# Performance work log

Hardware: AMD Instinct MI355X
Metric: run time of the kernel (lower is better)

Reference implementation:

```python
import jax, jax.numpy as jnp
import numpy as np

B, D, U = 64, 256, 256

def setup_inputs() -> dict:
    key = jax.random.key(0)
    ks = jax.random.split(key, 16)
    init_mu = 0.05
    inputs = jax.random.normal(ks[0], (B, D), jnp.float32)
    prev_state = 0.1 * jax.random.normal(ks[1], (B, U), jnp.float32)
    A = jax.random.normal(ks[2], (B, U, U), jnp.float32)
    # symmetric, diagonally boosted covariance-like state
    Sigma_state = 0.01 * (A + jnp.swapaxes(A, 1, 2)) + 0.1 * jnp.eye(U, dtype=jnp.float32)
    def w(k, shape):
        return init_mu * jax.random.normal(k, shape, jnp.float32)
    def s(k):
        return jax.random.uniform(k, (U,), jnp.float32, -4.5, -2.2)
    return {
        'inputs': inputs, 'prev_state': prev_state, 'Sigma_state': Sigma_state,
        'U_z': w(ks[3], (D, U)), 'uz_sigma': s(ks[4]), 'W_z': w(ks[5], (U, U)), 'wz_sigma': s(ks[6]),
        'U_r': w(ks[7], (D, U)), 'ur_sigma': s(ks[8]), 'W_r': w(ks[9], (U, U)), 'wr_sigma': s(ks[10]),
        'U_h': w(ks[11], (D, U)), 'uh_sigma': s(ks[12]), 'W_h': w(ks[13], (U, U)), 'wh_sigma': s(ks[14]),
    }

def _outer(a, b):  # [B,u],[B,u] -> [B,u,u]
    return a[:, :, None] * b[:, None, :]

def _quad(W, S):  # W^T @ S @ W, S is [B,u,u]
    return jnp.matmul(jnp.matmul(W.T, S), W)

def _x_sigma_w(x, sv):  # ||x||^2 * diag(softplus sigma)
    return jnp.sum(x * x, axis=1)[:, None, None] * jnp.diag(sv)

def _tr_sigma_w(S, sv):  # trace(S) * diag(softplus sigma)
    return jnp.trace(S, axis1=1, axis2=2)[:, None, None] * jnp.diag(sv)

def _hadamard_sigma(S1, S2, m1, m2):
    # S1*S2 + diag(m1) S2 diag(m1) + diag(m2) S1 diag(m2) as elementwise/broadcast
    return S1 * S2 + _outer(m1, m1) * S2 + _outer(m2, m2) * S1

def reference(inputs, prev_state, Sigma_state, U_z, uz_sigma, W_z, wz_sigma,
              U_r, ur_sigma, W_r, wr_sigma, U_h, uh_sigma, W_h, wh_sigma):
    sp = jax.nn.softplus
    # --- z gate ---
    az = inputs @ U_z + prev_state @ W_z
    z = jax.nn.sigmoid(az)
    gz = z * (1.0 - z)  # d sigmoid
    Sz = (_quad(W_z, Sigma_state) + _x_sigma_w(prev_state, sp(wz_sigma))
          + _tr_sigma_w(Sigma_state, sp(wz_sigma)) + _x_sigma_w(inputs, sp(uz_sigma)))
    Sigma_out_z = Sz * _outer(gz, gz)
    # --- r gate ---
    ar = inputs @ U_r + prev_state @ W_r
    r = jax.nn.sigmoid(ar)
    gr = r * (1.0 - r)
    Sr = (_quad(W_r, Sigma_state) + _x_sigma_w(prev_state, sp(wr_sigma))
          + _tr_sigma_w(Sigma_state, sp(wr_sigma)) + _x_sigma_w(inputs, sp(ur_sigma)))
    Sigma_out_r = Sr * _outer(gr, gr)
    # --- h candidate ---
    g_in = prev_state * r
    ah = inputs @ U_h + g_in @ W_h
    h = jnp.tanh(ah)
    gh = 1.0 - h * h  # d tanh
    sigma_g = _hadamard_sigma(Sigma_state, Sigma_out_r, prev_state, r)
    Sh = (_quad(W_h, sigma_g) + _x_sigma_w(g_in, sp(wh_sigma))
          + _tr_sigma_w(sigma_g, sp(wh_sigma)) + _x_sigma_w(inputs, sp(uh_sigma)))
    Sigma_out_h = Sh * _outer(gh, gh)
    # --- output combination ---
    mu_out = z * prev_state + (1.0 - z) * h
    sigma_a = _hadamard_sigma(Sigma_out_z, Sigma_state, z, prev_state)
    sigma_b = _hadamard_sigma(Sigma_out_z, Sigma_out_h, 1.0 - z, h)
    Sigma_out = (sigma_a + sigma_b
                 - Sigma_out_z * _outer(prev_state, h)
                 - Sigma_out_z * _outer(h, prev_state))
    Sigma_out = jnp.where(jnp.isnan(Sigma_out) | jnp.isinf(Sigma_out),
                          jnp.zeros_like(Sigma_out), Sigma_out)
    eye = jnp.eye(Sigma_out.shape[-1], dtype=Sigma_out.dtype)
    d = jnp.abs(jnp.diagonal(Sigma_out, axis1=1, axis2=2))
    Sigma_out = Sigma_out * (1.0 - eye) + d[:, :, None] * eye
    return mu_out, Sigma_out
```

## Files before the change

### kernel.cpp

```cpp
#include <hip/hip_runtime.h>
#include <math.h>

#define UDIM 256
#define BATCH 64
#define MATN 65536
#define PITCH 280

typedef __bf16 bf16x8 __attribute__((ext_vector_type(8)));
typedef float  f32x4  __attribute__((ext_vector_type(4)));

__device__ __forceinline__ float softplusf(float x) { return log1pf(expf(x)); }
__device__ __forceinline__ float sigmoidf_(float x) { return 1.f/(1.f+expf(-x)); }

__device__ __forceinline__ bf16x8 frag_load(const __bf16* base, int rt, int kt, int lane) {
  return *(const bf16x8*)(base + (((size_t)(rt*8 + kt))*64 + lane)*8);
}

__device__ __forceinline__ bf16x8 cvt8(const float* p) {
  const float4 f0 = *(const float4*)p;
  const float4 f1 = *(const float4*)(p + 4);
  bf16x8 v;
  v[0]=(__bf16)f0.x; v[1]=(__bf16)f0.y; v[2]=(__bf16)f0.z; v[3]=(__bf16)f0.w;
  v[4]=(__bf16)f1.x; v[5]=(__bf16)f1.y; v[6]=(__bf16)f1.z; v[7]=(__bf16)f1.w;
  return v;
}

__global__ __launch_bounds__(256) void prep_w(
    const float* __restrict__ Uz, const float* __restrict__ Wz,
    const float* __restrict__ Ur, const float* __restrict__ Wr,
    const float* __restrict__ Uh, const float* __restrict__ Wh,
    __bf16* __restrict__ Fu_z, __bf16* __restrict__ Fw_z,
    __bf16* __restrict__ Fu_r, __bf16* __restrict__ Fw_r,
    __bf16* __restrict__ Fu_h, __bf16* __restrict__ Fw_h,
    const float* __restrict__ S, const float* __restrict__ x,
    const float* __restrict__ prev, float* __restrict__ scal)
{
  const int u = blockIdx.x;
  const int t = threadIdx.x;
  if (u >= 96) {
    const int blk = u - 96;
    const int b = blk*4 + (t >> 6), l = t & 63;
    const float4 xv = *(const float4*)(x + b*UDIM + l*4);
    float s0 = xv.x*xv.x + xv.y*xv.y + xv.z*xv.z + xv.w*xv.w;
    const float4 pv = *(const float4*)(prev + b*UDIM + l*4);
    float s1 = pv.x*pv.x + pv.y*pv.y + pv.z*pv.z + pv.w*pv.w;
    float s2 = 0.f;
#pragma unroll
    for (int e = 0; e < 4; ++e)
      s2 += S[(size_t)b*MATN + (size_t)(l*4 + e)*257];
    for (int off = 32; off; off >>= 1) {
      s0 += __shfl_down(s0, off);
      s1 += __shfl_down(s1, off);
      s2 += __shfl_down(s2, off);
    }
    if (l == 0) {
      atomicAdd(&scal[b], s0);
      atomicAdd(&scal[64 + b], s1);
      atomicAdd(&scal[128 + b], s2);
    }
    return;
  }
  const int mat = u >> 4, tl = u & 15;
  const int n0 = (tl & 3)*64, k0 = (tl >> 2)*64;
  const float* W; __bf16* F;
  switch (mat) {
    case 0: W = Uz; F = Fu_z; break;  case 1: W = Wz; F = Fw_z; break;
    case 2: W = Ur; F = Fu_r; break;  case 3: W = Wr; F = Fw_r; break;
    case 4: W = Uh; F = Fu_h; break;  default: W = Wh; F = Fw_h; break;
  }
  __shared__ float tile[64][65];
  const int tx = t & 15, ty = t >> 4;
#pragma unroll
  for (int rr = 0; rr < 4; ++rr) {
    const int row = ty*4 + rr;
    const float4 f = *(const float4*)(W + (size_t)(k0 + row)*UDIM + n0 + tx*4);
    tile[row][tx*4+0] = f.x; tile[row][tx*4+1] = f.y;
    tile[row][tx*4+2] = f.z; tile[row][tx*4+3] = f.w;
  }
  __syncthreads();
#pragma unroll
  for (int ss = 0; ss < 2; ++ss) {
    const int s = t + ss*256;
    const int rt_l = s >> 7, kt_l = (s >> 6) & 1, lane = s & 63;
    const int nl = rt_l*16 + (lane & 15), kb = kt_l*32 + (lane >> 4)*8;
    __align__(16) __bf16 tmp[8];
#pragma unroll
    for (int e = 0; e < 8; ++e) tmp[e] = (__bf16)tile[kb + e][nl];
    *(uint4*)(F + (((size_t)((((n0 >> 4) + rt_l)*8) + (k0 >> 5) + kt_l))*64 + lane)*8)
        = *(const uint4*)tmp;
  }
}

__global__ __launch_bounds__(256) void sconv_gates(
    const float* __restrict__ S, __bf16* __restrict__ Sf,
    const float* __restrict__ x, const float* __restrict__ prev,
    const __bf16* __restrict__ Fu_z, const __bf16* __restrict__ Fw_z,
    const __bf16* __restrict__ Fu_r, const __bf16* __restrict__ Fw_r,
    float* __restrict__ zb, float* __restrict__ rb,
    float* __restrict__ gzb, float* __restrict__ grb,
    float* __restrict__ gin, float* __restrict__ scal)
{
  const int bid = blockIdx.x;
  const int t = threadIdx.x, w = t >> 6, l = t & 63, r = l & 15, q = l >> 4;

  if (bid < 8) {
    const int jt = bid & 3, gate = bid >> 2;
    const __bf16* FU = gate ? Fu_r : Fu_z;
    const __bf16* FW = gate ? Fw_r : Fw_z;
    const int mrow = w*16 + r;
    f32x4 acc[4] = {};
#pragma unroll
    for (int ks = 0; ks < 16; ++ks) {
      const int k0 = ks*32;
      const float* asrc; const __bf16* B; int kk;
      if (k0 < 256) { asrc = x    + (size_t)mrow*UDIM + k0         + q*8; B = FU; kk = k0; }
      else          { asrc = prev + (size_t)mrow*UDIM + (k0 - 256) + q*8; B = FW; kk = k0 - 256; }
      const bf16x8 af = cvt8(asrc);
#pragma unroll
      for (int ni = 0; ni < 4; ++ni) {
        const bf16x8 bv = frag_load(B, jt*4 + ni, kk >> 5, l);
        acc[ni] = __builtin_amdgcn_mfma_f32_16x16x32_bf16(af, bv, acc[ni], 0, 0, 0);
      }
    }
    if (gate == 0) {
#pragma unroll
      for (int ni = 0; ni < 4; ++ni) {
        const int n = jt*64 + ni*16 + r;
#pragma unroll
        for (int v = 0; v < 4; ++v) {
          const int m = w*16 + q*4 + v;
          const float zv = sigmoidf_(acc[ni][v]);
          zb[m*UDIM + n]  = zv;
          gzb[m*UDIM + n] = zv * (1.f - zv);
        }
      }
    } else {
      float ggp[4] = {0.f, 0.f, 0.f, 0.f};
#pragma unroll
      for (int ni = 0; ni < 4; ++ni) {
        const int n = jt*64 + ni*16 + r;
#pragma unroll
        for (int v = 0; v < 4; ++v) {
          const int m = w*16 + q*4 + v;
          const float rv = sigmoidf_(acc[ni][v]);
          const float pv = prev[m*UDIM + n];
          const float g2 = pv * rv;
          rb[m*UDIM + n]  = rv;
          grb[m*UDIM + n] = rv * (1.f - rv);
          gin[m*UDIM + n] = g2;
          ggp[v] += g2 * g2;
        }
      }
#pragma unroll
      for (int s = 1; s < 16; s <<= 1)
#pragma unroll
        for (int v = 0; v < 4; ++v) ggp[v] += __shfl_xor(ggp[v], s);
      if (r == 0)
#pragma unroll
        for (int v = 0; v < 4; ++v)
          atomicAdd(&scal[192 + w*16 + q*4 + v], ggp[v]);
    }
    return;
  }

  const int u = bid - 8;
  const int bx = u & 3, by = (u >> 2) & 3, b = u >> 4;
  const size_t sb = (size_t)b * MATN;
#pragma unroll
  for (int ss = 0; ss < 2; ++ss) {
    const int s = t + ss*256;
    const int chunk = s >> 6, lane = s & 63;
    const int rt_l = chunk >> 1, kt_l = chunk & 1;
    const int row = by*64 + rt_l*16 + (lane & 15);
    const int col = bx*64 + kt_l*32 + (lane >> 4)*8;
    const bf16x8 v = cvt8(S + sb + (size_t)row*UDIM + col);
    *(bf16x8*)(Sf + sb + (((size_t)((by*4 + rt_l)*8 + bx*2 + kt_l))*64 + lane)*8) = v;
  }
}

__global__ __launch_bounds__(256, 4) void quad_zr_gh(
    const float* __restrict__ S, const __bf16* __restrict__ Sf,
    const float* __restrict__ prev,
    const float* __restrict__ rb, const float* __restrict__ gzb,
    const float* __restrict__ grb,
    const float* __restrict__ wz_s, const float* __restrict__ uz_s,
    const float* __restrict__ wr_s, const float* __restrict__ ur_s,
    const __bf16* __restrict__ Fw_z, const __bf16* __restrict__ Fw_r,
    float* __restrict__ scal, __bf16* __restrict__ Szb, __bf16* __restrict__ G,
    const float* __restrict__ x, const float* __restrict__ gin,
    const float* __restrict__ zb,
    const __bf16* __restrict__ Fu_h, const __bf16* __restrict__ Fw_h,
    float* __restrict__ hb, float* __restrict__ ghb, float* __restrict__ mu_out)
{
  const int bid = blockIdx.x;
  const int t = threadIdx.x, w = t >> 6, l = t & 63, r = l & 15, q = l >> 4;

  if (bid < 4) {
    const int jt = bid;
    const int mrow = w*16 + r;
    f32x4 acc[4] = {};
#pragma unroll
    for (int ks = 0; ks < 16; ++ks) {
      const int k0 = ks*32;
      const float* asrc; const __bf16* B; int kk;
      if (k0 < 256) { asrc = x   + (size_t)mrow*UDIM + k0         + q*8; B = Fu_h; kk = k0; }
      else          { asrc = gin + (size_t)mrow*UDIM + (k0 - 256) + q*8; B = Fw_h; kk = k0 - 256; }
      const bf16x8 af = cvt8(asrc);
#pragma unroll
      for (int ni = 0; ni < 4; ++ni) {
        const bf16x8 bv = frag_load(B, jt*4 + ni, kk >> 5, l);
        acc[ni] = __builtin_amdgcn_mfma_f32_16x16x32_bf16(af, bv, acc[ni], 0, 0, 0);
      }
    }
#pragma unroll
    for (int ni = 0; ni < 4; ++ni) {
      const int n = jt*64 + ni*16 + r;
#pragma unroll
      for (int v = 0; v < 4; ++v) {
        const int m = w*16 + q*4 + v;
        const float hv = tanhf(acc[ni][v]);
        const float zv = zb[m*UDIM + n];
        hb[m*UDIM + n]  = hv;
        ghb[m*UDIM + n] = 1.f - hv*hv;
        mu_out[m*UDIM + n] = zv * prev[m*UDIM + n] + (1.f - zv) * hv;
      }
    }
    return;
  }

  const int id = bid - 4;
  const int gater = (id < 1024);
  const int rem = id & 1023;
  const int s = rem >> 6, b = rem & 63;
  const size_t sb = (size_t)b * MATN;
  const __bf16* Sfb = Sf + sb;
  const __bf16* FW = gater ? Fw_r : Fw_z;

  __shared__ __align__(16) __bf16 T[16*PITCH];

  f32x4 a[4] = {};
#pragma unroll
  for (int kt = 0; kt < 8; ++kt) {
    const bf16x8 af = frag_load(FW, s, kt, l);
#pragma unroll
    for (int ct = 0; ct < 4; ++ct) {
      const bf16x8 bv = frag_load(Sfb, w*4 + ct, kt, l);
      a[ct] = __builtin_amdgcn_mfma_f32_16x16x32_bf16(af, bv, a[ct], 0, 0, 0);
    }
  }
#pragma unroll
  for (int ct = 0; ct < 4; ++ct)
#pragma unroll
    for (int v = 0; v < 4; ++v)
      T[(q*4 + v)*PITCH + w*64 + ct*16 + r] = (__bf16)a[ct][v];
  __syncthreads();

  f32x4 qx[4] = {};
#pragma unroll
  for (int kt = 0; kt < 8; ++kt) {
    const bf16x8 at = *(const bf16x8*)&T[r*PITCH + kt*32 + q*8];
#pragma unroll
    for (int ct = 0; ct < 4; ++ct) {
      const bf16x8 bw = frag_load(FW, w*4 + ct, kt, l);
      qx[ct] = __builtin_amdgcn_mfma_f32_16x16x32_bf16(at, bw, qx[ct], 0, 0, 0);
    }
  }

  const float xx = scal[b];
  const float dscal = scal[64 + b] + scal[128 + b];
  const int ib = s*16 + q*4;

  if (!gater) {
    const f32x4 g4 = *(const f32x4*)(gzb + b*UDIM + ib);
    __align__(16) __bf16 o16[16];
#pragma unroll
    for (int ct = 0; ct < 4; ++ct) {
      const int j = (w*4 + ct)*16 + r;
      const float gj = gzb[b*UDIM + j];
#pragma unroll
      for (int v = 0; v < 4; ++v) {
        const int i = ib + v;
        float qv = qx[ct][v];
        if (i == j) qv += dscal*softplusf(wz_s[i]) + xx*softplusf(uz_s[i]);
        o16[ct*4 + v] = (__bf16)(qv * g4[v] * gj);
      }
    }
    __bf16* dst = Szb + ((size_t)(b*16 + s)*256 + t)*16;
    *(uint4*)dst       = *(const uint4*)&o16[0];
    *(uint4*)(dst + 8) = *(const uint4*)&o16[8];
  } else {
    float gvals[16];
    float trg = 0.f;
    {
      const f32x4 g4 = *(const f32x4*)(grb + b*UDIM + ib);
      const f32x4 p4 = *(const f32x4*)(prev + b*UDIM + ib);
      const f32x4 r4 = *(const f32x4*)(rb + b*UDIM + ib);
#pragma unroll
      for (int ct = 0; ct < 4; ++ct) {
        const int j = (w*4 + ct)*16 + r;
        const float gj = grb[b*UDIM + j];
        const float pj = prev[b*UDIM + j];
        const float rj = rb[b*UDIM + j];
#pragma unroll
        for (int v = 0; v < 4; ++v) {
          const int i = ib + v;
          float qv = qx[ct][v];
          if (i == j) qv += dscal*softplusf(wr_s[i]) + xx*softplusf(ur_s[i]);
          const float Sg = qv * g4[v] * gj;
          const float sv = S[sb + (size_t)i*UDIM + j];
          const float go = Sg*(sv + p4[v]*pj) + r4[v]*rj*sv;
          gvals[ct*4 + v] = go;
          if (i == j) trg += go;
        }
      }
    }
    if (trg != 0.f) atomicAdd(&scal[256 + b], trg);

    __syncthreads();
#pragma unroll
    for (int ct = 0; ct < 4; ++ct)
#pragma unroll
      for (int v = 0; v < 4; ++v)
        T[(q*4 + v)*PITCH + w*64 + ct*16 + r] = (__bf16)gvals[ct*4 + v];
    __syncthreads();
#pragma unroll
    for (int ee = 0; ee < 2; ++ee) {
      const int e = t + ee*256;
      const int kt = e >> 6, le = e & 63;
      const uint4 vv = *(const uint4*)&T[(le & 15)*PITCH + kt*32 + (le >> 4)*8];
      *(uint4*)(G + sb + (((size_t)(s*8 + kt))*64 + le)*8) = vv;
    }
  }
}

__global__ __launch_bounds__(256, 4) void quad_h(
    const float* __restrict__ S, const __bf16* __restrict__ Szb,
    const float* __restrict__ prev, const float* __restrict__ zb,
    const float* __restrict__ hb, const float* __restrict__ ghb,
    const float* __restrict__ wh_s, const float* __restrict__ uh_s,
    const __bf16* __restrict__ Fw_h, const __bf16* __restrict__ G,
    const float* __restrict__ scal, float* __restrict__ out_sig)
{
  const int bid = blockIdx.x;
  const int s = bid >> 6, b = bid & 63;
  const size_t sb = (size_t)b * MATN;
  const int t = threadIdx.x, w = t >> 6, l = t & 63, r = l & 15, q = l >> 4;
  const __bf16* Gb = G + sb;

  __shared__ __align__(16) __bf16 Th[16*PITCH];

  f32x4 ah[4] = {};
#pragma unroll
  for (int kt = 0; kt < 8; ++kt) {
    const bf16x8 af = frag_load(Fw_h, s, kt, l);
#pragma unroll
    for (int ct = 0; ct < 4; ++ct) {
      const bf16x8 bv = frag_load(Gb, w*4 + ct, kt, l);
      ah[ct] = __builtin_amdgcn_mfma_f32_16x16x32_bf16(af, bv, ah[ct], 0, 0, 0);
    }
  }
#pragma unroll
  for (int ct = 0; ct < 4; ++ct)
#pragma unroll
    for (int v = 0; v < 4; ++v)
      Th[(q*4 + v)*PITCH + w*64 + ct*16 + r] = (__bf16)ah[ct][v];
  __syncthreads();

  f32x4 qh[4] = {};
#pragma unroll
  for (int kt = 0; kt < 8; ++kt) {
    const bf16x8 at = *(const bf16x8*)&Th[r*PITCH + kt*32 + q*8];
#pragma unroll
    for (int ct = 0; ct < 4; ++ct) {
      const bf16x8 bv = frag_load(Fw_h, w*4 + ct, kt, l);
      qh[ct] = __builtin_amdgcn_mfma_f32_16x16x32_bf16(at, bv, qh[ct], 0, 0, 0);
    }
  }

  const float xx = scal[b];
  const float dscal = scal[192 + b] + scal[256 + b];
  const int ib = s*16 + q*4;

  const __bf16* szp = Szb + ((size_t)(b*16 + s)*256 + t)*16;
  __align__(16) __bf16 sz16[16];
  *(uint4*)&sz16[0] = *(const uint4*)szp;
  *(uint4*)&sz16[8] = *(const uint4*)(szp + 8);

  const f32x4 g4 = *(const f32x4*)(ghb + b*UDIM + ib);
  const f32x4 p4 = *(const f32x4*)(prev + b*UDIM + ib);
  const f32x4 z4 = *(const f32x4*)(zb + b*UDIM + ib);
  const f32x4 h4 = *(const f32x4*)(hb + b*UDIM + ib);

#pragma unroll
  for (int ct = 0; ct < 4; ++ct) {
    const int j = (w*4 + ct)*16 + r;
    const float gj = ghb[b*UDIM + j];
    const float pj = prev[b*UDIM + j];
    const float zj = zb[b*UDIM + j];
    const float hj = hb[b*UDIM + j];
#pragma unroll
    for (int v = 0; v < 4; ++v) {
      const int i = ib + v;
      float qv = qh[ct][v];
      if (i == j) qv += dscal*softplusf(wh_s[i]) + xx*softplusf(uh_s[i]);
      const float Sg = qv * g4[v] * gj;
      const float sv = S[sb + (size_t)i*UDIM + j];
      const float sz = (float)sz16[ct*4 + v];
      float val = sv*(sz + z4[v]*zj)
                + sz*(p4[v] - h4[v])*(pj - hj)
                + Sg*(sz + (1.f - z4[v])*(1.f - zj));
      if (!isfinite(val)) val = 0.f;
      if (i == j) val = fabsf(val);
      out_sig[sb + (size_t)i*UDIM + j] = val;
    }
  }
}

extern "C" void kernel_launch(void* const* d_in, const int* in_sizes, int n_in,
                              void* d_out, int out_size, void* d_ws, size_t ws_size,
                              hipStream_t stream) {
  const float* x    = (const float*)d_in[0];
  const float* prev = (const float*)d_in[1];
  const float* S    = (const float*)d_in[2];
  const float* Uz   = (const float*)d_in[3];
  const float* uz_s = (const float*)d_in[4];
  const float* Wz   = (const float*)d_in[5];
  const float* wz_s = (const float*)d_in[6];
  const float* Ur   = (const float*)d_in[7];
  const float* ur_s = (const float*)d_in[8];
  const float* Wr   = (const float*)d_in[9];
  const float* wr_s = (const float*)d_in[10];
  const float* Uh   = (const float*)d_in[11];
  const float* uh_s = (const float*)d_in[12];
  const float* Wh   = (const float*)d_in[13];
  const float* wh_s = (const float*)d_in[14];

  float* out_mu  = (float*)d_out;
  float* out_sig = out_mu + BATCH*UDIM;

  float* ws   = (float*)d_ws;
  float* zb   = ws;
  float* rb   = zb  + BATCH*UDIM;
  float* gzb  = rb  + BATCH*UDIM;
  float* grb  = gzb + BATCH*UDIM;
  float* gin  = grb + BATCH*UDIM;
  float* hb   = gin + BATCH*UDIM;
  float* ghb  = hb  + BATCH*UDIM;
  float* scal = ghb + BATCH*UDIM;
  __bf16* bws  = (__bf16*)(scal + 512);
  __bf16* Fu_z = bws;
  __bf16* Fw_z = Fu_z + MATN;
  __bf16* Fu_r = Fw_z + MATN;
  __bf16* Fw_r = Fu_r + MATN;
  __bf16* Fu_h = Fw_r + MATN;
  __bf16* Fw_h = Fu_h + MATN;
  const size_t BIG = (size_t)BATCH * MATN;
  __bf16* Szb = Fw_h + MATN;
  __bf16* G   = Szb + BIG;
  __bf16* Sf  = G + BIG;

  hipMemsetAsync(scal, 0, 512*sizeof(float), stream);

  prep_w<<<dim3(112), 256, 0, stream>>>(Uz, Wz, Ur, Wr, Uh, Wh,
      Fu_z, Fw_z, Fu_r, Fw_r, Fu_h, Fw_h, S, x, prev, scal);
  sconv_gates<<<dim3(1032), 256, 0, stream>>>(S, Sf, x, prev,
      Fu_z, Fw_z, Fu_r, Fw_r, zb, rb, gzb, grb, gin, scal);
  quad_zr_gh<<<dim3(2052), 256, 0, stream>>>(S, Sf, prev, rb, gzb, grb,
      wz_s, uz_s, wr_s, ur_s, Fw_z, Fw_r, scal, Szb, G,
      x, gin, zb, Fu_h, Fw_h, hb, ghb, out_mu);
  quad_h<<<dim3(1024), 256, 0, stream>>>(S, Szb, prev, zb, hb, ghb,
      wh_s, uh_s, Fw_h, G, scal, out_sig);
}
```

Measured before the change: 166.3 us.

## Batch multiple row-strips per block in quad kernels and split gate GEMM

Moves the Sigma bf16 fragment conversion into the prep kernel and splits the z/r gate GEMM into 32 small blocks with one output tile each. The quad kernels now compute 4 (zr) or 2 (h) row strips per block, so each loaded Sigma/G fragment feeds several MFMAs. The shared scratch tile is also reused to stage the G output instead of a register array. This cuts redundant global loads of S fragments and the number of launched blocks, at the cost of more registers and LDS per block and lower occupancy (launch bounds lowered to 2).

Measured after the change: 172.0 us. 3.4% more time.

```diff
diff --git a/kernel.cpp b/kernel.cpp
--- a/kernel.cpp
+++ b/kernel.cpp
@@ -33,10 +33,27 @@
     __bf16* __restrict__ Fu_r, __bf16* __restrict__ Fw_r,
     __bf16* __restrict__ Fu_h, __bf16* __restrict__ Fw_h,
     const float* __restrict__ S, const float* __restrict__ x,
-    const float* __restrict__ prev, float* __restrict__ scal)
+    const float* __restrict__ prev, float* __restrict__ scal,
+    __bf16* __restrict__ Sf)
 {
   const int u = blockIdx.x;
   const int t = threadIdx.x;
+  if (u >= 112) {
+    const int c = u - 112;
+    const int bx = c & 3, by = (c >> 2) & 3, b = c >> 4;
+    const size_t sb = (size_t)b * MATN;
+#pragma unroll
+    for (int ss = 0; ss < 2; ++ss) {
+      const int s = t + ss*256;
+      const int chunk = s >> 6, lane = s & 63;
+      const int rt_l = chunk >> 1, kt_l = chunk & 1;
+      const int row = by*64 + rt_l*16 + (lane & 15);
+      const int col = bx*64 + kt_l*32 + (lane >> 4)*8;
+      const bf16x8 v = cvt8(S + sb + (size_t)row*UDIM + col);
+      *(bf16x8*)(Sf + sb + (((size_t)((by*4 + rt_l)*8 + bx*2 + kt_l))*64 + lane)*8) = v;
+    }
+    return;
+  }
   if (u >= 96) {
     const int blk = u - 96;
     const int b = blk*4 + (t >> 6), l = t & 63;
@@ -91,8 +108,7 @@
   }
 }
 
-__global__ __launch_bounds__(256) void sconv_gates(
-    const float* __restrict__ S, __bf16* __restrict__ Sf,
+__global__ __launch_bounds__(256) void gates_zr(
     const float* __restrict__ x, const float* __restrict__ prev,
     const __bf16* __restrict__ Fu_z, const __bf16* __restrict__ Fw_z,
     const __bf16* __restrict__ Fu_r, const __bf16* __restrict__ Fw_r,
@@ -101,84 +117,56 @@
     float* __restrict__ gin, float* __restrict__ scal)
 {
   const int bid = blockIdx.x;
+  const int gate = bid >> 4, jt = (bid >> 2) & 3, ni = bid & 3;
   const int t = threadIdx.x, w = t >> 6, l = t & 63, r = l & 15, q = l >> 4;
-
-  if (bid < 8) {
-    const int jt = bid & 3, gate = bid >> 2;
-    const __bf16* FU = gate ? Fu_r : Fu_z;
-    const __bf16* FW = gate ? Fw_r : Fw_z;
-    const int mrow = w*16 + r;
-    f32x4 acc[4] = {};
-#pragma unroll
-    for (int ks = 0; ks < 16; ++ks) {
-      const int k0 = ks*32;
-      const float* asrc; const __bf16* B; int kk;
-      if (k0 < 256) { asrc = x    + (size_t)mrow*UDIM + k0         + q*8; B = FU; kk = k0; }
-      else          { asrc = prev + (size_t)mrow*UDIM + (k0 - 256) + q*8; B = FW; kk = k0 - 256; }
-      const bf16x8 af = cvt8(asrc);
-#pragma unroll
-      for (int ni = 0; ni < 4; ++ni) {
-        const bf16x8 bv = frag_load(B, jt*4 + ni, kk >> 5, l);
-        acc[ni] = __builtin_amdgcn_mfma_f32_16x16x32_bf16(af, bv, acc[ni], 0, 0, 0);
-      }
-    }
-    if (gate == 0) {
-#pragma unroll
-      for (int ni = 0; ni < 4; ++ni) {
-        const int n = jt*64 + ni*16 + r;
-#pragma unroll
-        for (int v = 0; v < 4; ++v) {
-          const int m = w*16 + q*4 + v;
-          const float zv = sigmoidf_(acc[ni][v]);
-          zb[m*UDIM + n]  = zv;
-          gzb[m*UDIM + n] = zv * (1.f - zv);
-        }
-      }
-    } else {
-      float ggp[4] = {0.f, 0.f, 0.f, 0.f};
-#pragma unroll
-      for (int ni = 0; ni < 4; ++ni) {
-        const int n = jt*64 + ni*16 + r;
-#pragma unroll
-        for (int v = 0; v < 4; ++v) {
-          const int m = w*16 + q*4 + v;
-          const float rv = sigmoidf_(acc[ni][v]);
-          const float pv = prev[m*UDIM + n];
-          const float g2 = pv * rv;
-          rb[m*UDIM + n]  = rv;
-          grb[m*UDIM + n] = rv * (1.f - rv);
-          gin[m*UDIM + n] = g2;
-          ggp[v] += g2 * g2;
-        }
-      }
-#pragma unroll
-      for (int s = 1; s < 16; s <<= 1)
-#pragma unroll
-        for (int v = 0; v < 4; ++v) ggp[v] += __shfl_xor(ggp[v], s);
-      if (r == 0)
-#pragma unroll
-        for (int v = 0; v < 4; ++v)
-          atomicAdd(&scal[192 + w*16 + q*4 + v], ggp[v]);
-    }
-    return;
-  }
-
-  const int u = bid - 8;
-  const int bx = u & 3, by = (u >> 2) & 3, b = u >> 4;
-  const size_t sb = (size_t)b * MATN;
-#pragma unroll
-  for (int ss = 0; ss < 2; ++ss) {
-    const int s = t + ss*256;
-    const int chunk = s >> 6, lane = s & 63;
-    const int rt_l = chunk >> 1, kt_l = chunk & 1;
-    const int row = by*64 + rt_l*16 + (lane & 15);
-    const int col = bx*64 + kt_l*32 + (lane >> 4)*8;
-    const bf16x8 v = cvt8(S + sb + (size_t)row*UDIM + col);
-    *(bf16x8*)(Sf + sb + (((size_t)((by*4 + rt_l)*8 + bx*2 + kt_l))*64 + lane)*8) = v;
-  }
-}
-
-__global__ __launch_bounds__(256, 4) void quad_zr_gh(
+  const __bf16* FU = gate ? Fu_r : Fu_z;
+  const __bf16* FW = gate ? Fw_r : Fw_z;
+  const int mrow = w*16 + r;
+  f32x4 acc = {};
+#pragma unroll
+  for (int ks = 0; ks < 16; ++ks) {
+    const int k0 = ks*32;
+    const float* asrc; const __bf16* B; int kk;
+    if (k0 < 256) { asrc = x    + (size_t)mrow*UDIM + k0         + q*8; B = FU; kk = k0; }
+    else          { asrc = prev + (size_t)mrow*UDIM + (k0 - 256) + q*8; B = FW; kk = k0 - 256; }
+    const bf16x8 af = cvt8(asrc);
+    const bf16x8 bv = frag_load(B, jt*4 + ni, kk >> 5, l);
+    acc = __builtin_amdgcn_mfma_f32_16x16x32_bf16(af, bv, acc, 0, 0, 0);
+  }
+  const int n = jt*64 + ni*16 + r;
+  if (gate == 0) {
+#pragma unroll
+    for (int v = 0; v < 4; ++v) {
+      const int m = w*16 + q*4 + v;
+      const float zv = sigmoidf_(acc[v]);
+      zb[m*UDIM + n]  = zv;
+      gzb[m*UDIM + n] = zv * (1.f - zv);
+    }
+  } else {
+    float ggp[4];
+#pragma unroll
+    for (int v = 0; v < 4; ++v) {
+      const int m = w*16 + q*4 + v;
+      const float rv = sigmoidf_(acc[v]);
+      const float pv = prev[m*UDIM + n];
+      const float g2 = pv * rv;
+      rb[m*UDIM + n]  = rv;
+      grb[m*UDIM + n] = rv * (1.f - rv);
+      gin[m*UDIM + n] = g2;
+      ggp[v] = g2 * g2;
+    }
+#pragma unroll
+    for (int s = 1; s < 16; s <<= 1)
+#pragma unroll
+      for (int v = 0; v < 4; ++v) ggp[v] += __shfl_xor(ggp[v], s);
+    if (r == 0)
+#pragma unroll
+      for (int v = 0; v < 4; ++v)
+        atomicAdd(&scal[192 + w*16 + q*4 + v], ggp[v]);
+  }
+}
+
+__global__ __launch_bounds__(256, 2) void quad_zr_gh(
     const float* __restrict__ S, const __bf16* __restrict__ Sf,
     const float* __restrict__ prev,
     const float* __restrict__ rb, const float* __restrict__ gzb,
@@ -229,69 +217,86 @@
   }
 
   const int id = bid - 4;
-  const int gater = (id < 1024);
-  const int rem = id & 1023;
-  const int s = rem >> 6, b = rem & 63;
+  const int gater = (id < 256);
+  const int rem = id & 255;
+  const int sg = rem >> 6, b = rem & 63;
   const size_t sb = (size_t)b * MATN;
   const __bf16* Sfb = Sf + sb;
   const __bf16* FW = gater ? Fw_r : Fw_z;
 
-  __shared__ __align__(16) __bf16 T[16*PITCH];
-
-  f32x4 a[4] = {};
+  __shared__ __align__(16) __bf16 T[4*16*PITCH];
+
+  f32x4 a[4][4] = {};
 #pragma unroll
   for (int kt = 0; kt < 8; ++kt) {
-    const bf16x8 af = frag_load(FW, s, kt, l);
+    bf16x8 af[4];
+#pragma unroll
+    for (int sl = 0; sl < 4; ++sl) af[sl] = frag_load(FW, sg*4 + sl, kt, l);
 #pragma unroll
     for (int ct = 0; ct < 4; ++ct) {
       const bf16x8 bv = frag_load(Sfb, w*4 + ct, kt, l);
-      a[ct] = __builtin_amdgcn_mfma_f32_16x16x32_bf16(af, bv, a[ct], 0, 0, 0);
-    }
-  }
-#pragma unroll
-  for (int ct = 0; ct < 4; ++ct)
-#pragma unroll
-    for (int v = 0; v < 4; ++v)
-      T[(q*4 + v)*PITCH + w*64 + ct*16 + r] = (__bf16)a[ct][v];
+#pragma unroll
+      for (int sl = 0; sl < 4; ++sl)
+        a[sl][ct] = __builtin_amdgcn_mfma_f32_16x16x32_bf16(af[sl], bv, a[sl][ct], 0, 0, 0);
+    }
+  }
+#pragma unroll
+  for (int sl = 0; sl < 4; ++sl)
+#pragma unroll
+    for (int ct = 0; ct < 4; ++ct)
+#pragma unroll
+      for (int v = 0; v < 4; ++v)
+        T[sl*16*PITCH + (q*4 + v)*PITCH + w*64 + ct*16 + r] = (__bf16)a[sl][ct][v];
   __syncthreads();
 
-  f32x4 qx[4] = {};
+  f32x4 qx[4][4] = {};
 #pragma unroll
   for (int kt = 0; kt < 8; ++kt) {
-    const bf16x8 at = *(const bf16x8*)&T[r*PITCH + kt*32 + q*8];
-#pragma unroll
-    for (int ct = 0; ct < 4; ++ct) {
-      const bf16x8 bw = frag_load(FW, w*4 + ct, kt, l);
-      qx[ct] = __builtin_amdgcn_mfma_f32_16x16x32_bf16(at, bw, qx[ct], 0, 0, 0);
+    bf16x8 bw[4];
+#pragma unroll
+    for (int ct = 0; ct < 4; ++ct) bw[ct] = frag_load(FW, w*4 + ct, kt, l);
+#pragma unroll
+    for (int sl = 0; sl < 4; ++sl) {
+      const bf16x8 at = *(const bf16x8*)&T[sl*16*PITCH + r*PITCH + kt*32 + q*8];
+#pragma unroll
+      for (int ct = 0; ct < 4; ++ct)
+        qx[sl][ct] = __builtin_amdgcn_mfma_f32_16x16x32_bf16(at, bw[ct], qx[sl][ct], 0, 0, 0);
     }
   }
 
   const float xx = scal[b];
   const float dscal = scal[64 + b] + scal[128 + b];
-  const int ib = s*16 + q*4;
 
   if (!gater) {
-    const f32x4 g4 = *(const f32x4*)(gzb + b*UDIM + ib);
-    __align__(16) __bf16 o16[16];
-#pragma unroll
-    for (int ct = 0; ct < 4; ++ct) {
-      const int j = (w*4 + ct)*16 + r;
-      const float gj = gzb[b*UDIM + j];
-#pragma unroll
-      for (int v = 0; v < 4; ++v) {
-        const int i = ib + v;
-        float qv = qx[ct][v];
-        if (i == j) qv += dscal*softplusf(wz_s[i]) + xx*softplusf(uz_s[i]);
-        o16[ct*4 + v] = (__bf16)(qv * g4[v] * gj);
-      }
-    }
-    __bf16* dst = Szb + ((size_t)(b*16 + s)*256 + t)*16;
-    *(uint4*)dst       = *(const uint4*)&o16[0];
-    *(uint4*)(dst + 8) = *(const uint4*)&o16[8];
+#pragma unroll
+    for (int sl = 0; sl < 4; ++sl) {
+      const int s4 = sg*4 + sl;
+      const int ib = s4*16 + q*4;
+      const f32x4 g4 = *(const f32x4*)(gzb + b*UDIM + ib);
+      __align__(16) __bf16 o16[16];
+#pragma unroll
+      for (int ct = 0; ct < 4; ++ct) {
+        const int j = (w*4 + ct)*16 + r;
+        const float gj = gzb[b*UDIM + j];
+#pragma unroll
+        for (int v = 0; v < 4; ++v) {
+          const int i = ib + v;
+          float qv = qx[sl][ct][v];
+          if (i == j) qv += dscal*softplusf(wz_s[i]) + xx*softplusf(uz_s[i]);
+          o16[ct*4 + v] = (__bf16)(qv * g4[v] * gj);
+        }
+      }
+      __bf16* dst = Szb + ((size_t)(b*16 + s4)*256 + t)*16;
+      *(uint4*)dst       = *(const uint4*)&o16[0];
+      *(uint4*)(dst + 8) = *(const uint4*)&o16[8];
+    }
   } else {
-    float gvals[16];
+    __syncthreads();
     float trg = 0.f;
-    {
+#pragma unroll
+    for (int sl = 0; sl < 4; ++sl) {
+      const int s4 = sg*4 + sl;
+      const int ib = s4*16 + q*4;
       const f32x4 g4 = *(const f32x4*)(grb + b*UDIM + ib);
       const f32x4 p4 = *(const f32x4*)(prev + b*UDIM + ib);
       const f32x4 r4 = *(const f32x4*)(rb + b*UDIM + ib);
@@ -304,36 +309,31 @@
 #pragma unroll
         for (int v = 0; v < 4; ++v) {
           const int i = ib + v;
-          float qv = qx[ct][v];
+          float qv = qx[sl][ct][v];
           if (i == j) qv += dscal*softplusf(wr_s[i]) + xx*softplusf(ur_s[i]);
           const float Sg = qv * g4[v] * gj;
           const float sv = S[sb + (size_t)i*UDIM + j];
           const float go = Sg*(sv + p4[v]*pj) + r4[v]*rj*sv;
-          gvals[ct*4 + v] = go;
+          T[sl*16*PITCH + (q*4 + v)*PITCH + w*64 + ct*16 + r] = (__bf16)go;
           if (i == j) trg += go;
         }
       }
     }
     if (trg != 0.f) atomicAdd(&scal[256 + b], trg);
-
     __syncthreads();
 #pragma unroll
-    for (int ct = 0; ct < 4; ++ct)
-#pragma unroll
-      for (int v = 0; v < 4; ++v)
-        T[(q*4 + v)*PITCH + w*64 + ct*16 + r] = (__bf16)gvals[ct*4 + v];
-    __syncthreads();
-#pragma unroll
-    for (int ee = 0; ee < 2; ++ee) {
-      const int e = t + ee*256;
-      const int kt = e >> 6, le = e & 63;
-      const uint4 vv = *(const uint4*)&T[(le & 15)*PITCH + kt*32 + (le >> 4)*8];
-      *(uint4*)(G + sb + (((size_t)(s*8 + kt))*64 + le)*8) = vv;
-    }
-  }
-}
-
-__global__ __launch_bounds__(256, 4) void quad_h(
+    for (int sl = 0; sl < 4; ++sl)
+#pragma unroll
+      for (int ee = 0; ee < 2; ++ee) {
+        const int e = t + ee*256;
+        const int kt = e >> 6, le = e & 63;
+        const uint4 vv = *(const uint4*)&T[sl*16*PITCH + (le & 15)*PITCH + kt*32 + (le >> 4)*8];
+        *(uint4*)(G + sb + (((size_t)((sg*4 + sl)*8 + kt))*64 + le)*8) = vv;
+      }
+  }
+}
+
+__global__ __launch_bounds__(256, 2) void quad_h(
     const float* __restrict__ S, const __bf16* __restrict__ Szb,
     const float* __restrict__ prev, const float* __restrict__ zb,
     const float* __restrict__ hb, const float* __restrict__ ghb,
@@ -342,76 +342,91 @@
     const float* __restrict__ scal, float* __restrict__ out_sig)
 {
   const int bid = blockIdx.x;
-  const int s = bid >> 6, b = bid & 63;
+  const int sg = bid >> 6, b = bid & 63;
   const size_t sb = (size_t)b * MATN;
   const int t = threadIdx.x, w = t >> 6, l = t & 63, r = l & 15, q = l >> 4;
   const __bf16* Gb = G + sb;
 
-  __shared__ __align__(16) __bf16 Th[16*PITCH];
-
-  f32x4 ah[4] = {};
+  __shared__ __align__(16) __bf16 Th[2*16*PITCH];
+
+  f32x4 ah[2][4] = {};
 #pragma unroll
   for (int kt = 0; kt < 8; ++kt) {
-    const bf16x8 af = frag_load(Fw_h, s, kt, l);
+    bf16x8 af[2];
+#pragma unroll
+    for (int sl = 0; sl < 2; ++sl) af[sl] = frag_load(Fw_h, sg*2 + sl, kt, l);
 #pragma unroll
     for (int ct = 0; ct < 4; ++ct) {
       const bf16x8 bv = frag_load(Gb, w*4 + ct, kt, l);
-      ah[ct] = __builtin_amdgcn_mfma_f32_16x16x32_bf16(af, bv, ah[ct], 0, 0, 0);
-    }
-  }
-#pragma unroll
-  for (int ct = 0; ct < 4; ++ct)
-#pragma unroll
-    for (int v = 0; v < 4; ++v)
-      Th[(q*4 + v)*PITCH + w*64 + ct*16 + r] = (__bf16)ah[ct][v];
+#pragma unroll
+      for (int sl = 0; sl < 2; ++sl)
+        ah[sl][ct] = __builtin_amdgcn_mfma_f32_16x16x32_bf16(af[sl], bv, ah[sl][ct], 0, 0, 0);
+    }
+  }
+#pragma unroll
+  for (int sl = 0; sl < 2; ++sl)
+#pragma unroll
+    for (int ct = 0; ct < 4; ++ct)
+#pragma unroll
+      for (int v = 0; v < 4; ++v)
+        Th[sl*16*PITCH + (q*4 + v)*PITCH + w*64 + ct*16 + r] = (__bf16)ah[sl][ct][v];
   __syncthreads();
 
-  f32x4 qh[4] = {};
+  f32x4 qh[2][4] = {};
 #pragma unroll
   for (int kt = 0; kt < 8; ++kt) {
-    const bf16x8 at = *(const bf16x8*)&Th[r*PITCH + kt*32 + q*8];
-#pragma unroll
-    for (int ct = 0; ct < 4; ++ct) {
-      const bf16x8 bv = frag_load(Fw_h, w*4 + ct, kt, l);
-      qh[ct] = __builtin_amdgcn_mfma_f32_16x16x32_bf16(at, bv, qh[ct], 0, 0, 0);
+    bf16x8 bw[4];
+#pragma unroll
+    for (int ct = 0; ct < 4; ++ct) bw[ct] = frag_load(Fw_h, w*4 + ct, kt, l);
+#pragma unroll
+    for (int sl = 0; sl < 2; ++sl) {
+      const bf16x8 at = *(const bf16x8*)&Th[sl*16*PITCH + r*PITCH + kt*32 + q*8];
+#pragma unroll
+      for (int ct = 0; ct < 4; ++ct)
+        qh[sl][ct] = __builtin_amdgcn_mfma_f32_16x16x32_bf16(at, bw[ct], qh[sl][ct], 0, 0, 0);
     }
   }
 
   const float xx = scal[b];
   const float dscal = scal[192 + b] + scal[256 + b];
-  const int ib = s*16 + q*4;
-
-  const __bf16* szp = Szb + ((size_t)(b*16 + s)*256 + t)*16;
-  __align__(16) __bf16 sz16[16];
-  *(uint4*)&sz16[0] = *(const uint4*)szp;
-  *(uint4*)&sz16[8] = *(const uint4*)(szp + 8);
-
-  const f32x4 g4 = *(const f32x4*)(ghb + b*UDIM + ib);
-  const f32x4 p4 = *(const f32x4*)(prev + b*UDIM + ib);
-  const f32x4 z4 = *(const f32x4*)(zb + b*UDIM + ib);
-  const f32x4 h4 = *(const f32x4*)(hb + b*UDIM + ib);
-
-#pragma unroll
-  for (int ct = 0; ct < 4; ++ct) {
-    const int j = (w*4 + ct)*16 + r;
-    const float gj = ghb[b*UDIM + j];
-    const float pj = prev[b*UDIM + j];
-    const float zj = zb[b*UDIM + j];
-    const float hj = hb[b*UDIM + j];
-#pragma unroll
-    for (int v = 0; v < 4; ++v) {
-      const int i = ib + v;
-      float qv = qh[ct][v];
-      if (i == j) qv += dscal*softplusf(wh_s[i]) + xx*softplusf(uh_s[i]);
-      const float Sg = qv * g4[v] * gj;
-      const float sv = S[sb + (size_t)i*UDIM + j];
-      const float sz = (float)sz16[ct*4 + v];
-      float val = sv*(sz + z4[v]*zj)
-                + sz*(p4[v] - h4[v])*(pj - hj)
-                + Sg*(sz + (1.f - z4[v])*(1.f - zj));
-      if (!isfinite(val)) val = 0.f;
-      if (i == j) val = fabsf(val);
-      out_sig[sb + (size_t)i*UDIM + j] = val;
+
+#pragma unroll
+  for (int sl = 0; sl < 2; ++sl) {
+    const int s4 = sg*2 + sl;
+    const int ib = s4*16 + q*4;
+
+    const __bf16* szp = Szb + ((size_t)(b*16 + s4)*256 + t)*16;
+    __align__(16) __bf16 sz16[16];
+    *(uint4*)&sz16[0] = *(const uint4*)szp;
+    *(uint4*)&sz16[8] = *(const uint4*)(szp + 8);
+
+    const f32x4 g4 = *(const f32x4*)(ghb + b*UDIM + ib);
+    const f32x4 p4 = *(const f32x4*)(prev + b*UDIM + ib);
+    const f32x4 z4 = *(const f32x4*)(zb + b*UDIM + ib);
+    const f32x4 h4 = *(const f32x4*)(hb + b*UDIM + ib);
+
+#pragma unroll
+    for (int ct = 0; ct < 4; ++ct) {
+      const int j = (w*4 + ct)*16 + r;
+      const float gj = ghb[b*UDIM + j];
+      const float pj = prev[b*UDIM + j];
+      const float zj = zb[b*UDIM + j];
+      const float hj = hb[b*UDIM + j];
+#pragma unroll
+      for (int v = 0; v < 4; ++v) {
+        const int i = ib + v;
+        float qv = qh[sl][ct][v];
+        if (i == j) qv += dscal*softplusf(wh_s[i]) + xx*softplusf(uh_s[i]);
+        const float Sg = qv * g4[v] * gj;
+        const float sv = S[sb + (size_t)i*UDIM + j];
+        const float sz = (float)sz16[ct*4 + v];
+        float val = sv*(sz + z4[v]*zj)
+                  + sz*(p4[v] - h4[v])*(pj - hj)
+                  + Sg*(sz + (1.f - z4[v])*(1.f - zj));
+        if (!isfinite(val)) val = 0.f;
+        if (i == j) val = fabsf(val);
+        out_sig[sb + (size_t)i*UDIM + j] = val;
+      }
     }
   }
 }
@@ -461,13 +476,13 @@
 
   hipMemsetAsync(scal, 0, 512*sizeof(float), stream);
 
-  prep_w<<<dim3(112), 256, 0, stream>>>(Uz, Wz, Ur, Wr, Uh, Wh,
-      Fu_z, Fw_z, Fu_r, Fw_r, Fu_h, Fw_h, S, x, prev, scal);
-  sconv_gates<<<dim3(1032), 256, 0, stream>>>(S, Sf, x, prev,
+  prep_w<<<dim3(1136), 256, 0, stream>>>(Uz, Wz, Ur, Wr, Uh, Wh,
+      Fu_z, Fw_z, Fu_r, Fw_r, Fu_h, Fw_h, S, x, prev, scal, Sf);
+  gates_zr<<<dim3(32), 256, 0, stream>>>(x, prev,
       Fu_z, Fw_z, Fu_r, Fw_r, zb, rb, gzb, grb, gin, scal);
-  quad_zr_gh<<<dim3(2052), 256, 0, stream>>>(S, Sf, prev, rb, gzb, grb,
+  quad_zr_gh<<<dim3(516), 256, 0, stream>>>(S, Sf, prev, rb, gzb, grb,
       wz_s, uz_s, wr_s, ur_s, Fw_z, Fw_r, scal, Szb, G,
       x, gin, zb, Fu_h, Fw_h, hb, ghb, out_mu);
-  quad_h<<<dim3(1024), 256, 0, stream>>>(S, Szb, prev, zb, hb, ghb,
+  quad_h<<<dim3(512), 256, 0, stream>>>(S, Szb, prev, zb, hb, ghb,
       wh_s, uh_s, Fw_h, G, scal, out_sig);
 }
```

## Merge weight prep, S conversion and z/r gate GEMMs into one kernel

Applied to the files above, without the earlier changes.

Merges the prep_w and sconv_gates launches into a single prep_all kernel, which removes one launch and its dependency barrier. The z/r gate GEMM no longer waits for pre-swizzled Fu_z/Fw_z/Fu_r/Fw_r fragments. Each gate block now loads its 16-column slice of the raw fp32 U/W matrices, converts it to bf16 in LDS, and computes one 16-wide output tile, so 32 small blocks replace 8 larger ones. The scalar-norm blocks store their sums directly instead of using atomics. This trades redundant weight reads and a larger LDS footprint per block for a shorter critical path at the start.

Measured after the change: 166.0 us. No clear change (-0.2%).

```diff
diff --git a/kernel.cpp b/kernel.cpp
--- a/kernel.cpp
+++ b/kernel.cpp
@@ -25,156 +25,164 @@
   return v;
 }
 
-__global__ __launch_bounds__(256) void prep_w(
+__global__ __launch_bounds__(256) void prep_all(
     const float* __restrict__ Uz, const float* __restrict__ Wz,
     const float* __restrict__ Ur, const float* __restrict__ Wr,
     const float* __restrict__ Uh, const float* __restrict__ Wh,
-    __bf16* __restrict__ Fu_z, __bf16* __restrict__ Fw_z,
-    __bf16* __restrict__ Fu_r, __bf16* __restrict__ Fw_r,
+    __bf16* __restrict__ Fw_z, __bf16* __restrict__ Fw_r,
     __bf16* __restrict__ Fu_h, __bf16* __restrict__ Fw_h,
     const float* __restrict__ S, const float* __restrict__ x,
-    const float* __restrict__ prev, float* __restrict__ scal)
+    const float* __restrict__ prev, float* __restrict__ scal,
+    __bf16* __restrict__ Sf,
+    float* __restrict__ zb, float* __restrict__ rb,
+    float* __restrict__ gzb, float* __restrict__ grb,
+    float* __restrict__ gin)
 {
-  const int u = blockIdx.x;
+  const int bid = blockIdx.x;
   const int t = threadIdx.x;
-  if (u >= 96) {
-    const int blk = u - 96;
-    const int b = blk*4 + (t >> 6), l = t & 63;
-    const float4 xv = *(const float4*)(x + b*UDIM + l*4);
+  const int w = t >> 6, l = t & 63, r = l & 15, q = l >> 4;
+
+  __shared__ __align__(16) unsigned char LDSU[16896];
+
+  if (bid < 1024) {
+    const int c = bid;
+    const int bx = c & 3, by = (c >> 2) & 3, b = c >> 4;
+    const size_t sb = (size_t)b * MATN;
+#pragma unroll
+    for (int ss = 0; ss < 2; ++ss) {
+      const int s = t + ss*256;
+      const int chunk = s >> 6, lane = s & 63;
+      const int rt_l = chunk >> 1, kt_l = chunk & 1;
+      const int row = by*64 + rt_l*16 + (lane & 15);
+      const int col = bx*64 + kt_l*32 + (lane >> 4)*8;
+      const bf16x8 v = cvt8(S + sb + (size_t)row*UDIM + col);
+      *(bf16x8*)(Sf + sb + (((size_t)((by*4 + rt_l)*8 + bx*2 + kt_l))*64 + lane)*8) = v;
+    }
+    return;
+  }
+
+  if (bid < 1088) {
+    const int u3 = bid - 1024;
+    const int mat = u3 >> 4, tl = u3 & 15;
+    const int n0 = (tl & 3)*64, k0 = (tl >> 2)*64;
+    const float* W; __bf16* F;
+    switch (mat) {
+      case 0: W = Wz; F = Fw_z; break;  case 1: W = Wr; F = Fw_r; break;
+      case 2: W = Uh; F = Fu_h; break;  default: W = Wh; F = Fw_h; break;
+    }
+    float (*tile)[65] = (float (*)[65])LDSU;
+    const int tx = t & 15, ty = t >> 4;
+#pragma unroll
+    for (int rr = 0; rr < 4; ++rr) {
+      const int row = ty*4 + rr;
+      const float4 f = *(const float4*)(W + (size_t)(k0 + row)*UDIM + n0 + tx*4);
+      tile[row][tx*4+0] = f.x; tile[row][tx*4+1] = f.y;
+      tile[row][tx*4+2] = f.z; tile[row][tx*4+3] = f.w;
+    }
+    __syncthreads();
+#pragma unroll
+    for (int ss = 0; ss < 2; ++ss) {
+      const int s = t + ss*256;
+      const int rt_l = s >> 7, kt_l = (s >> 6) & 1, lane = s & 63;
+      const int nl = rt_l*16 + (lane & 15), kb = kt_l*32 + (lane >> 4)*8;
+      __align__(16) __bf16 tmp[8];
+#pragma unroll
+      for (int e = 0; e < 8; ++e) tmp[e] = (__bf16)tile[kb + e][nl];
+      *(uint4*)(F + (((size_t)((((n0 >> 4) + rt_l)*8) + (k0 >> 5) + kt_l))*64 + lane)*8)
+          = *(const uint4*)tmp;
+    }
+    return;
+  }
+
+  if (bid < 1104) {
+    const int blk = bid - 1088;
+    const int b0 = blk*4 + (t >> 6);
+    const float4 xv = *(const float4*)(x + b0*UDIM + l*4);
     float s0 = xv.x*xv.x + xv.y*xv.y + xv.z*xv.z + xv.w*xv.w;
-    const float4 pv = *(const float4*)(prev + b*UDIM + l*4);
+    const float4 pv = *(const float4*)(prev + b0*UDIM + l*4);
     float s1 = pv.x*pv.x + pv.y*pv.y + pv.z*pv.z + pv.w*pv.w;
     float s2 = 0.f;
 #pragma unroll
     for (int e = 0; e < 4; ++e)
-      s2 += S[(size_t)b*MATN + (size_t)(l*4 + e)*257];
+      s2 += S[(size_t)b0*MATN + (size_t)(l*4 + e)*257];
     for (int off = 32; off; off >>= 1) {
       s0 += __shfl_down(s0, off);
       s1 += __shfl_down(s1, off);
       s2 += __shfl_down(s2, off);
     }
-    if (l == 0) {
-      atomicAdd(&scal[b], s0);
-      atomicAdd(&scal[64 + b], s1);
-      atomicAdd(&scal[128 + b], s2);
-    }
+    if (l == 0) { scal[b0] = s0; scal[64 + b0] = s1; scal[128 + b0] = s2; }
     return;
   }
-  const int mat = u >> 4, tl = u & 15;
-  const int n0 = (tl & 3)*64, k0 = (tl >> 2)*64;
-  const float* W; __bf16* F;
-  switch (mat) {
-    case 0: W = Uz; F = Fu_z; break;  case 1: W = Wz; F = Fw_z; break;
-    case 2: W = Ur; F = Fu_r; break;  case 3: W = Wr; F = Fw_r; break;
-    case 4: W = Uh; F = Fu_h; break;  default: W = Wh; F = Fw_h; break;
-  }
-  __shared__ float tile[64][65];
-  const int tx = t & 15, ty = t >> 4;
-#pragma unroll
-  for (int rr = 0; rr < 4; ++rr) {
-    const int row = ty*4 + rr;
-    const float4 f = *(const float4*)(W + (size_t)(k0 + row)*UDIM + n0 + tx*4);
-    tile[row][tx*4+0] = f.x; tile[row][tx*4+1] = f.y;
-    tile[row][tx*4+2] = f.z; tile[row][tx*4+3] = f.w;
-  }
-  __syncthreads();
-#pragma unroll
-  for (int ss = 0; ss < 2; ++ss) {
-    const int s = t + ss*256;
-    const int rt_l = s >> 7, kt_l = (s >> 6) & 1, lane = s & 63;
-    const int nl = rt_l*16 + (lane & 15), kb = kt_l*32 + (lane >> 4)*8;
-    __align__(16) __bf16 tmp[8];
-#pragma unroll
-    for (int e = 0; e < 8; ++e) tmp[e] = (__bf16)tile[kb + e][nl];
-    *(uint4*)(F + (((size_t)((((n0 >> 4) + rt_l)*8) + (k0 >> 5) + kt_l))*64 + lane)*8)
-        = *(const uint4*)tmp;
-  }
-}
-
-__global__ __launch_bounds__(256) void sconv_gates(
-    const float* __restrict__ S, __bf16* __restrict__ Sf,
-    const float* __restrict__ x, const float* __restrict__ prev,
-    const __bf16* __restrict__ Fu_z, const __bf16* __restrict__ Fw_z,
-    const __bf16* __restrict__ Fu_r, const __bf16* __restrict__ Fw_r,
-    float* __restrict__ zb, float* __restrict__ rb,
-    float* __restrict__ gzb, float* __restrict__ grb,
-    float* __restrict__ gin, float* __restrict__ scal)
-{
-  const int bid = blockIdx.x;
-  const int t = threadIdx.x, w = t >> 6, l = t & 63, r = l & 15, q = l >> 4;
-
-  if (bid < 8) {
-    const int jt = bid & 3, gate = bid >> 2;
-    const __bf16* FU = gate ? Fu_r : Fu_z;
-    const __bf16* FW = gate ? Fw_r : Fw_z;
+
+  {
+    const int u2 = bid - 1104;
+    const int g = u2 >> 4, un = u2 & 15;
+    const int jt = un >> 2, ni = un & 3;
+    const int n0 = un * 16;
+    const float* Um = g ? Ur : Uz;
+    const float* Wm = g ? Wr : Wz;
+    __bf16 (*Ut)[16][264] = (__bf16 (*)[16][264])LDSU;
+    {
+      float uv[16], wv[16];
+      const float* ur_ = Um + (size_t)t*UDIM + n0;
+      const float* wr_ = Wm + (size_t)t*UDIM + n0;
+#pragma unroll
+      for (int p4 = 0; p4 < 4; ++p4) {
+        *(float4*)&uv[p4*4] = *(const float4*)(ur_ + p4*4);
+        *(float4*)&wv[p4*4] = *(const float4*)(wr_ + p4*4);
+      }
+#pragma unroll
+      for (int e = 0; e < 16; ++e) {
+        Ut[0][e][t] = (__bf16)uv[e];
+        Ut[1][e][t] = (__bf16)wv[e];
+      }
+    }
+    __syncthreads();
+
     const int mrow = w*16 + r;
-    f32x4 acc[4] = {};
+    f32x4 acc = {};
 #pragma unroll
     for (int ks = 0; ks < 16; ++ks) {
       const int k0 = ks*32;
-      const float* asrc; const __bf16* B; int kk;
-      if (k0 < 256) { asrc = x    + (size_t)mrow*UDIM + k0         + q*8; B = FU; kk = k0; }
-      else          { asrc = prev + (size_t)mrow*UDIM + (k0 - 256) + q*8; B = FW; kk = k0 - 256; }
+      const float* asrc;
+      int src, koff;
+      if (k0 < 256) { asrc = x    + (size_t)mrow*UDIM + k0         + q*8; src = 0; koff = k0; }
+      else          { asrc = prev + (size_t)mrow*UDIM + (k0 - 256) + q*8; src = 1; koff = k0 - 256; }
       const bf16x8 af = cvt8(asrc);
-#pragma unroll
-      for (int ni = 0; ni < 4; ++ni) {
-        const bf16x8 bv = frag_load(B, jt*4 + ni, kk >> 5, l);
-        acc[ni] = __builtin_amdgcn_mfma_f32_16x16x32_bf16(af, bv, acc[ni], 0, 0, 0);
-      }
-    }
-    if (gate == 0) {
-#pragma unroll
-      for (int ni = 0; ni < 4; ++ni) {
-        const int n = jt*64 + ni*16 + r;
-#pragma unroll
-        for (int v = 0; v < 4; ++v) {
-          const int m = w*16 + q*4 + v;
-          const float zv = sigmoidf_(acc[ni][v]);
-          zb[m*UDIM + n]  = zv;
-          gzb[m*UDIM + n] = zv * (1.f - zv);
-        }
+      const bf16x8 bv = *(const bf16x8*)&Ut[src][r][koff + q*8];
+      acc = __builtin_amdgcn_mfma_f32_16x16x32_bf16(af, bv, acc, 0, 0, 0);
+    }
+    const int n = n0 + r;
+    if (g == 0) {
+#pragma unroll
+      for (int v = 0; v < 4; ++v) {
+        const int m = w*16 + q*4 + v;
+        const float zv = sigmoidf_(acc[v]);
+        zb[m*UDIM + n]  = zv;
+        gzb[m*UDIM + n] = zv * (1.f - zv);
       }
     } else {
-      float ggp[4] = {0.f, 0.f, 0.f, 0.f};
-#pragma unroll
-      for (int ni = 0; ni < 4; ++ni) {
-        const int n = jt*64 + ni*16 + r;
-#pragma unroll
-        for (int v = 0; v < 4; ++v) {
-          const int m = w*16 + q*4 + v;
-          const float rv = sigmoidf_(acc[ni][v]);
-          const float pv = prev[m*UDIM + n];
-          const float g2 = pv * rv;
-          rb[m*UDIM + n]  = rv;
-          grb[m*UDIM + n] = rv * (1.f - rv);
-          gin[m*UDIM + n] = g2;
-          ggp[v] += g2 * g2;
-        }
-      }
-#pragma unroll
-      for (int s = 1; s < 16; s <<= 1)
-#pragma unroll
-        for (int v = 0; v < 4; ++v) ggp[v] += __shfl_xor(ggp[v], s);
+      float ggp[4];
+#pragma unroll
+      for (int v = 0; v < 4; ++v) {
+        const int m = w*16 + q*4 + v;
+        const float rv = sigmoidf_(acc[v]);
+        const float pv = prev[m*UDIM + n];
+        const float g2 = pv * rv;
+        rb[m*UDIM + n]  = rv;
+        grb[m*UDIM + n] = rv * (1.f - rv);
+        gin[m*UDIM + n] = g2;
+        ggp[v] = g2 * g2;
+      }
+#pragma unroll
+      for (int s2 = 1; s2 < 16; s2 <<= 1)
+#pragma unroll
+        for (int v = 0; v < 4; ++v) ggp[v] += __shfl_xor(ggp[v], s2);
       if (r == 0)
 #pragma unroll
         for (int v = 0; v < 4; ++v)
           atomicAdd(&scal[192 + w*16 + q*4 + v], ggp[v]);
     }
-    return;
-  }
-
-  const int u = bid - 8;
-  const int bx = u & 3, by = (u >> 2) & 3, b = u >> 4;
-  const size_t sb = (size_t)b * MATN;
-#pragma unroll
-  for (int ss = 0; ss < 2; ++ss) {
-    const int s = t + ss*256;
-    const int chunk = s >> 6, lane = s & 63;
-    const int rt_l = chunk >> 1, kt_l = chunk & 1;
-    const int row = by*64 + rt_l*16 + (lane & 15);
-    const int col = bx*64 + kt_l*32 + (lane >> 4)*8;
-    const bf16x8 v = cvt8(S + sb + (size_t)row*UDIM + col);
-    *(bf16x8*)(Sf + sb + (((size_t)((by*4 + rt_l)*8 + bx*2 + kt_l))*64 + lane)*8) = v;
   }
 }
 
@@ -459,12 +467,11 @@
   __bf16* G   = Szb + BIG;
   __bf16* Sf  = G + BIG;
 
-  hipMemsetAsync(scal, 0, 512*sizeof(float), stream);
-
-  prep_w<<<dim3(112), 256, 0, stream>>>(Uz, Wz, Ur, Wr, Uh, Wh,
-      Fu_z, Fw_z, Fu_r, Fw_r, Fu_h, Fw_h, S, x, prev, scal);
-  sconv_gates<<<dim3(1032), 256, 0, stream>>>(S, Sf, x, prev,
-      Fu_z, Fw_z, Fu_r, Fw_r, zb, rb, gzb, grb, gin, scal);
+  (void)hipMemsetAsync(scal, 0, 512*sizeof(float), stream);
+
+  prep_all<<<dim3(1136), 256, 0, stream>>>(Uz, Wz, Ur, Wr, Uh, Wh,
+      Fw_z, Fw_r, Fu_h, Fw_h, S, x, prev, scal, Sf,
+      zb, rb, gzb, grb, gin);
   quad_zr_gh<<<dim3(2052), 256, 0, stream>>>(S, Sf, prev, rb, gzb, grb,
       wz_s, uz_s, wr_s, ur_s, Fw_z, Fw_r, scal, Szb, G,
       x, gin, zb, Fu_h, Fw_h, hb, ghb, out_mu);
```
